# Kernel optimization log

Measured on AMD Instinct MI355X. Metric: run time of the kernel, lower is better.

## Reference

```python
import jax, jax.numpy as jnp
import numpy as np

B = 1024          # batch
IMG_IN = 4096     # raw visual feature dim
AUD_IN = 1024     # raw audio feature dim
ENC = 1024        # encoder output dim
S = 3             # multi-scale branches (768 = 3*256 in out_layer)
D = 256           # MmFA feature dim (hardcoded in module)
OUT1 = 512
LAT = 128         # minus_one_dim
NCLS = 10
NORM = 1.0 / np.sqrt(256.0)  # note: original applies this AFTER softmax


def setup_inputs() -> dict:
    key = jax.random.key(0)
    ks = jax.random.split(key, 16)
    n = lambda k, shape, s=0.02: jax.random.normal(k, shape, dtype=jnp.float32) * s
    return dict(
        img=jax.random.normal(ks[0], (B, IMG_IN), dtype=jnp.float32),
        audio=jax.random.normal(ks[1], (B, AUD_IN), dtype=jnp.float32),
        vis_W=n(ks[2], (ENC, IMG_IN)), vis_b=jnp.zeros((ENC,), jnp.float32),
        aud_W=n(ks[3], (ENC, AUD_IN)), aud_b=jnp.zeros((ENC,), jnp.float32),
        msv_W=n(ks[4], (S, D, ENC)), msv_b=jnp.zeros((S, D), jnp.float32),
        msa_W=n(ks[5], (S, D, ENC)), msa_b=jnp.zeros((S, D), jnp.float32),
        mmfa_W=n(ks[6], (8, D, D)),  # q_v,q_a,k_v,k_a,w1,w2,w3,w4
        mmfa_b=jnp.zeros((8, D), jnp.float32),
        bil_W=n(ks[7], (D, D, D)),   # nn.Bilinear(256,256,256,bias=False)
        t_c=jnp.ones((), jnp.float32),
        out_W1=n(ks[8], (OUT1, S * D)), out_b1=jnp.zeros((OUT1,), jnp.float32),
        out_W2=n(ks[9], (LAT, OUT1)), out_b2=jnp.zeros((LAT,), jnp.float32),
        clsv_W1=n(ks[10], (32, LAT)), clsv_W2=n(ks[11], (NCLS, 32)),
        clsa_W1=n(ks[12], (32, LAT)), clsa_W2=n(ks[13], (NCLS, 32)),
    )


def _mmfa(x_v, x_a, W, b, bil_W, t_c):
    # x_v, x_a: [B, S, D]
    lin = lambda i, x: jnp.einsum('bsd,kd->bsk', x, W[i]) + b[i]
    q_v, q_a, k_v, k_a = lin(0, x_v), lin(1, x_a), lin(2, x_v), lin(3, x_a)
    # faithful to source: softmax first, then scale by 1/sqrt(dim_k)
    att = lambda q, k: jax.nn.softmax(jnp.einsum('bsd,btd->bst', q, k), axis=-1) * NORM
    alpha_va = jnp.einsum('bst,btd->bsd', att(q_v, k_a), x_a)
    alpha_v = jnp.einsum('bst,btd->bsd', att(q_v, k_v), x_v)
    alpha_av = jnp.einsum('bst,btd->bsd', att(q_a, k_v), x_v)
    alpha_a = jnp.einsum('bst,btd->bsd', att(q_a, k_a), x_a)
    c_va = jax.nn.sigmoid((lin(4, alpha_va) + lin(5, alpha_v)) * alpha_v)
    c_av = jax.nn.sigmoid((lin(6, alpha_av) + lin(7, alpha_a)) * alpha_a)
    j = jax.nn.sigmoid(jnp.einsum('bsi,oij,bsj->bso', c_va, bil_W, c_av))
    return t_c * j * x_v + (1.0 - j) * x_a


def reference(img, audio, vis_W, vis_b, aud_W, aud_b, msv_W, msv_b, msa_W, msa_b,
              mmfa_W, mmfa_b, bil_W, t_c, out_W1, out_b1, out_W2, out_b2,
              clsv_W1, clsv_W2, clsa_W1, clsa_W2):
    vis = jax.nn.relu(img @ vis_W.T + vis_b)       # [B, ENC]
    aud = jax.nn.relu(audio @ aud_W.T + aud_b)     # [B, ENC]
    # reconstructed MultiScale_Modal_Net: 3 parallel Linear(ENC->D)+ReLU -> [B,S,D]
    v_ms = jax.nn.relu(jnp.einsum('bd,skd->bsk', vis, msv_W) + msv_b)
    a_ms = jax.nn.relu(jnp.einsum('bd,skd->bsk', aud, msa_W) + msa_b)
    M1 = _mmfa(v_ms, a_ms, mmfa_W, mmfa_b, bil_W, t_c)
    M2 = _mmfa(M1 * v_ms, M1 * a_ms, mmfa_W, mmfa_b, bil_W, t_c)
    ov = (M2 * v_ms).reshape(img.shape[0], -1)     # [B, 768]
    oa = (M2 * a_ms).reshape(img.shape[0], -1)
    # out_layer (dropout = identity in eval)
    fv = jax.nn.relu(ov @ out_W1.T + out_b1) @ out_W2.T + out_b2   # [B, 128]
    fa = jax.nn.relu(oa @ out_W1.T + out_b1) @ out_W2.T + out_b2
    pv = jax.nn.relu(fv @ clsv_W1.T) @ clsv_W2.T                   # [B, 10]
    pa = jax.nn.relu(fa @ clsa_W1.T) @ clsa_W2.T
    return (fv, fa, pv, pa)
```

## Files before the change

kernel.cpp:

```cpp
#include <hip/hip_runtime.h>
#include <math.h>


typedef short short8   __attribute__((ext_vector_type(8)));
typedef float floatx4  __attribute__((ext_vector_type(4)));

constexpr float NORM = 0.0625f;

__device__ __forceinline__ unsigned short f2bf(float f) {
    union { float f; unsigned int u; } v; v.f = f;
    unsigned int r = v.u + 0x7fffu + ((v.u >> 16) & 1u);
    return (unsigned short)(r >> 16);
}
__device__ __forceinline__ float bf2f(unsigned short s) {
    union { unsigned int u; float f; } v; v.u = ((unsigned int)s) << 16;
    return v.f;
}

template<int ACT>
__global__ __launch_bounds__(256)
void gemm_mfma(const float* __restrict__ A, const unsigned short* __restrict__ W,
               const float* __restrict__ bias, float* __restrict__ C,
               int M, int N, int K)
{
    __shared__ short sA[64][72];
    __shared__ short sW[64][72];
    const int tid  = threadIdx.x;
    const int wave = tid >> 6, lane = tid & 63;
    const int quad = lane >> 4, l15 = lane & 15;
    const int m0 = blockIdx.y * 64, n0 = blockIdx.x * 64;
    const int mw = (wave & 1) * 32, nw = (wave >> 1) * 32;
    const int srow = tid >> 2, sseg = tid & 3;

    floatx4 P[2][2];
    #pragma unroll
    for (int f = 0; f < 2; f++)
        #pragma unroll
        for (int g = 0; g < 2; g++)
            P[f][g] = (floatx4){0.f, 0.f, 0.f, 0.f};

    for (int k0 = 0; k0 < K; k0 += 64) {
        const float* ap = A + (size_t)(m0 + srow) * K + k0 + sseg * 16;
        float4 a0 = *(const float4*)(ap);
        float4 a1 = *(const float4*)(ap + 4);
        float4 a2 = *(const float4*)(ap + 8);
        float4 a3 = *(const float4*)(ap + 12);
        union { unsigned short s[8]; short8 v; } p0, p1;
        p0.s[0] = f2bf(a0.x); p0.s[1] = f2bf(a0.y); p0.s[2] = f2bf(a0.z); p0.s[3] = f2bf(a0.w);
        p0.s[4] = f2bf(a1.x); p0.s[5] = f2bf(a1.y); p0.s[6] = f2bf(a1.z); p0.s[7] = f2bf(a1.w);
        p1.s[0] = f2bf(a2.x); p1.s[1] = f2bf(a2.y); p1.s[2] = f2bf(a2.z); p1.s[3] = f2bf(a2.w);
        p1.s[4] = f2bf(a3.x); p1.s[5] = f2bf(a3.y); p1.s[6] = f2bf(a3.z); p1.s[7] = f2bf(a3.w);
        *(short8*)&sA[srow][sseg * 16]     = p0.v;
        *(short8*)&sA[srow][sseg * 16 + 8] = p1.v;
        const unsigned short* wp = W + (size_t)(n0 + srow) * K + k0 + sseg * 16;
        *(short8*)&sW[srow][sseg * 16]     = *(const short8*)wp;
        *(short8*)&sW[srow][sseg * 16 + 8] = *(const short8*)(wp + 8);
        __syncthreads();
        #pragma unroll
        for (int kh = 0; kh < 2; kh++) {
            short8 af[2], wf[2];
            af[0] = *(short8*)&sA[mw + l15][kh * 32 + quad * 8];
            af[1] = *(short8*)&sA[mw + 16 + l15][kh * 32 + quad * 8];
            wf[0] = *(short8*)&sW[nw + l15][kh * 32 + quad * 8];
            wf[1] = *(short8*)&sW[nw + 16 + l15][kh * 32 + quad * 8];
            #pragma unroll
            for (int f = 0; f < 2; f++)
                #pragma unroll
                for (int g = 0; g < 2; g++)
                    P[f][g] = __builtin_amdgcn_mfma_f32_16x16x32_bf16(af[f], wf[g], P[f][g], 0, 0, 0);
        }
        __syncthreads();
    }
    #pragma unroll
    for (int f = 0; f < 2; f++)
        #pragma unroll
        for (int g = 0; g < 2; g++)
            #pragma unroll
            for (int r = 0; r < 4; r++) {
                int m = m0 + mw + 16 * f + quad * 4 + r;
                int n = n0 + nw + 16 * g + l15;
                float v = P[f][g][r] + bias[n];
                if (ACT) v = fmaxf(v, 0.f);
                C[(size_t)m * N + n] = v;
            }
}

__global__ __launch_bounds__(256)
void gemm_sigm(const float* __restrict__ A, const unsigned short* __restrict__ W,
               const float* __restrict__ bias, const float* __restrict__ al,
               unsigned short* __restrict__ Cbf, int M, int N, int K)
{
    __shared__ short sA[64][72];
    __shared__ short sW[64][72];
    const int tid  = threadIdx.x;
    const int wave = tid >> 6, lane = tid & 63;
    const int quad = lane >> 4, l15 = lane & 15;
    const int m0 = blockIdx.y * 64, n0 = blockIdx.x * 64;
    const int mw = (wave & 1) * 32, nw = (wave >> 1) * 32;
    const int srow = tid >> 2, sseg = tid & 3;

    floatx4 P[2][2];
    #pragma unroll
    for (int f = 0; f < 2; f++)
        #pragma unroll
        for (int g = 0; g < 2; g++)
            P[f][g] = (floatx4){0.f, 0.f, 0.f, 0.f};

    for (int k0 = 0; k0 < K; k0 += 64) {
        const float* ap = A + (size_t)(m0 + srow) * K + k0 + sseg * 16;
        float4 a0 = *(const float4*)(ap);
        float4 a1 = *(const float4*)(ap + 4);
        float4 a2 = *(const float4*)(ap + 8);
        float4 a3 = *(const float4*)(ap + 12);
        union { unsigned short s[8]; short8 v; } p0, p1;
        p0.s[0] = f2bf(a0.x); p0.s[1] = f2bf(a0.y); p0.s[2] = f2bf(a0.z); p0.s[3] = f2bf(a0.w);
        p0.s[4] = f2bf(a1.x); p0.s[5] = f2bf(a1.y); p0.s[6] = f2bf(a1.z); p0.s[7] = f2bf(a1.w);
        p1.s[0] = f2bf(a2.x); p1.s[1] = f2bf(a2.y); p1.s[2] = f2bf(a2.z); p1.s[3] = f2bf(a2.w);
        p1.s[4] = f2bf(a3.x); p1.s[5] = f2bf(a3.y); p1.s[6] = f2bf(a3.z); p1.s[7] = f2bf(a3.w);
        *(short8*)&sA[srow][sseg * 16]     = p0.v;
        *(short8*)&sA[srow][sseg * 16 + 8] = p1.v;
        const unsigned short* wp = W + (size_t)(n0 + srow) * K + k0 + sseg * 16;
        *(short8*)&sW[srow][sseg * 16]     = *(const short8*)wp;
        *(short8*)&sW[srow][sseg * 16 + 8] = *(const short8*)(wp + 8);
        __syncthreads();
        #pragma unroll
        for (int kh = 0; kh < 2; kh++) {
            short8 af[2], wf[2];
            af[0] = *(short8*)&sA[mw + l15][kh * 32 + quad * 8];
            af[1] = *(short8*)&sA[mw + 16 + l15][kh * 32 + quad * 8];
            wf[0] = *(short8*)&sW[nw + l15][kh * 32 + quad * 8];
            wf[1] = *(short8*)&sW[nw + 16 + l15][kh * 32 + quad * 8];
            #pragma unroll
            for (int f = 0; f < 2; f++)
                #pragma unroll
                for (int g = 0; g < 2; g++)
                    P[f][g] = __builtin_amdgcn_mfma_f32_16x16x32_bf16(af[f], wf[g], P[f][g], 0, 0, 0);
        }
        __syncthreads();
    }
    #pragma unroll
    for (int f = 0; f < 2; f++)
        #pragma unroll
        for (int g = 0; g < 2; g++)
            #pragma unroll
            for (int r = 0; r < 4; r++) {
                int m = m0 + mw + 16 * f + quad * 4 + r;
                int n = n0 + nw + 16 * g + l15;
                float v = P[f][g][r] + bias[n];
                float a = al[(size_t)m * 512 + 256 + n];
                Cbf[(size_t)m * N + n] = f2bf(1.f / (1.f + expf(-v * a)));
            }
}

template<int ACT>
__global__ __launch_bounds__(256)
void gemm_bt(const float* __restrict__ A, const float* __restrict__ W,
             const float* __restrict__ bias, float* __restrict__ C,
             int M, int N, int K)
{
    __shared__ __align__(16) float sA[32][68];
    __shared__ __align__(16) float sB[32][68];
    const int tid = threadIdx.x;
    const int m0 = blockIdx.y * 64;
    const int n0 = blockIdx.x * 64;
    const int tx = tid & 15;
    const int ty = tid >> 4;
    const int kk = tid & 31;
    const int rr = tid >> 5;
    float acc[4][4] = {};
    for (int k0 = 0; k0 < K; k0 += 32) {
        #pragma unroll
        for (int p = 0; p < 8; p++) {
            int mm = rr + p * 8;
            int m  = m0 + mm;
            int k  = k0 + kk;
            sA[kk][mm] = (m < M && k < K) ? A[(size_t)m * K + k] : 0.f;
        }
        #pragma unroll
        for (int p = 0; p < 8; p++) {
            int nn = rr + p * 8;
            int n  = n0 + nn;
            int k  = k0 + kk;
            sB[kk][nn] = (n < N && k < K) ? W[(size_t)n * K + k] : 0.f;
        }
        __syncthreads();
        #pragma unroll
        for (int q = 0; q < 32; q++) {
            float av[4], bv[4];
            #pragma unroll
            for (int i = 0; i < 4; i++) av[i] = sA[q][ty * 4 + i];
            #pragma unroll
            for (int j = 0; j < 4; j++) bv[j] = sB[q][tx * 4 + j];
            #pragma unroll
            for (int i = 0; i < 4; i++)
                #pragma unroll
                for (int j = 0; j < 4; j++)
                    acc[i][j] += av[i] * bv[j];
        }
        __syncthreads();
    }
    #pragma unroll
    for (int i = 0; i < 4; i++) {
        int m = m0 + ty * 4 + i;
        if (m >= M) continue;
        #pragma unroll
        for (int j = 0; j < 4; j++) {
            int n = n0 + tx * 4 + j;
            if (n >= N) continue;
            float v = acc[i][j];
            if (bias) v += bias[n];
            if (ACT) v = fmaxf(v, 0.f);
            C[(size_t)m * N + n] = v;
        }
    }
}

__global__ __launch_bounds__(256)
void conv_w(const float* __restrict__ src, unsigned short* __restrict__ dst, int n)
{
    int i = (blockIdx.x * 256 + threadIdx.x) * 8;
    if (i + 7 < n) {
        float4 a = *(const float4*)(src + i);
        float4 b = *(const float4*)(src + i + 4);
        union { unsigned short s[8]; uint4 v; } o;
        o.s[0] = f2bf(a.x); o.s[1] = f2bf(a.y); o.s[2] = f2bf(a.z); o.s[3] = f2bf(a.w);
        o.s[4] = f2bf(b.x); o.s[5] = f2bf(b.y); o.s[6] = f2bf(b.z); o.s[7] = f2bf(b.w);
        *(uint4*)(dst + i) = o.v;
    }
}

__global__ __launch_bounds__(256)
void pack_kcat(const float* __restrict__ mW, unsigned short* __restrict__ Wcva,
               unsigned short* __restrict__ Wcav)
{
    int i = blockIdx.x * 256 + threadIdx.x;
    int row = i >> 8, col = i & 255;
    Wcva[row * 512 + col]       = f2bf(mW[4 * 65536 + i]);
    Wcva[row * 512 + 256 + col] = f2bf(mW[5 * 65536 + i]);
    Wcav[row * 512 + col]       = f2bf(mW[6 * 65536 + i]);
    Wcav[row * 512 + 256 + col] = f2bf(mW[7 * 65536 + i]);
}

__global__ __launch_bounds__(256)
void pack_bias(const float* __restrict__ mb, float* __restrict__ bqkv,
               float* __restrict__ bqka, float* __restrict__ bcva,
               float* __restrict__ bcav)
{
    int i = blockIdx.x * 256 + threadIdx.x;
    int c = i & 255;
    bqkv[i] = mb[(i < 256 ? 0 : 512) + c];
    bqka[i] = mb[(i < 256 ? 256 : 768) + c];
    if (i < 256) {
        bcva[i] = mb[4 * 256 + i] + mb[5 * 256 + i];
        bcav[i] = mb[6 * 256 + i] + mb[7 * 256 + i];
    }
}

__global__ __launch_bounds__(512, 4)
void bilinear_col(const unsigned short* __restrict__ cav,
                  const unsigned short* __restrict__ cva,
                  const float* __restrict__ Wf,
                  float* __restrict__ outT)
{
    __shared__ short sA[64][264];
    __shared__ float sRed[8][64];
    const int tid  = threadIdx.x;
    const int wave = tid >> 6, lane = tid & 63;
    const int quad = lane >> 4, l15 = lane & 15;
    const int o     = blockIdx.x;
    const int mbase = blockIdx.y * 1536;
    const int i0    = wave * 32;

    short8 Wr[2][8];
    {
        const float* wo = Wf + (size_t)o * 65536;
        #pragma unroll
        for (int f = 0; f < 2; f++) {
            const float* wrow = wo + (size_t)(i0 + 16 * f + l15) * 256 + quad * 8;
            #pragma unroll
            for (int s = 0; s < 8; s++) {
                float4 lo = *(const float4*)(wrow + s * 32);
                float4 hi = *(const float4*)(wrow + s * 32 + 4);
                union { unsigned short u[8]; short8 v; } p;
                p.u[0] = f2bf(lo.x); p.u[1] = f2bf(lo.y); p.u[2] = f2bf(lo.z); p.u[3] = f2bf(lo.w);
                p.u[4] = f2bf(hi.x); p.u[5] = f2bf(hi.y); p.u[6] = f2bf(hi.z); p.u[7] = f2bf(hi.w);
                Wr[f][s] = p.v;
            }
        }
    }

    const int srow = tid >> 3, sseg = tid & 7;
    for (int ms = 0; ms < 24; ms++) {
        const int m0 = mbase + ms * 64;
        __syncthreads();
        {
            const unsigned short* src = cav + (size_t)(m0 + srow) * 256 + sseg * 32;
            #pragma unroll
            for (int u = 0; u < 4; u++)
                *(short8*)&sA[srow][sseg * 32 + u * 8] = *(const short8*)(src + u * 8);
        }
        __syncthreads();

        uint2 raws[2][4];
        #pragma unroll
        for (int g = 0; g < 4; g++)
            #pragma unroll
            for (int f = 0; f < 2; f++)
                raws[f][g] = *(const uint2*)(cva + (size_t)(m0 + 16 * g + l15) * 256
                                                  + i0 + 16 * f + 4 * quad);

        floatx4 P2[2][4];
        #pragma unroll
        for (int f = 0; f < 2; f++)
            #pragma unroll
            for (int g = 0; g < 4; g++)
                P2[f][g] = (floatx4){0.f, 0.f, 0.f, 0.f};

        #pragma unroll
        for (int s = 0; s < 8; s++) {
            short8 bg[4];
            #pragma unroll
            for (int g = 0; g < 4; g++)
                bg[g] = *(const short8*)&sA[16 * g + l15][s * 32 + quad * 8];
            #pragma unroll
            for (int f = 0; f < 2; f++)
                #pragma unroll
                for (int g = 0; g < 4; g++)
                    P2[f][g] = __builtin_amdgcn_mfma_f32_16x16x32_bf16(Wr[f][s], bg[g], P2[f][g], 0, 0, 0);
        }

        float T[4] = {0.f, 0.f, 0.f, 0.f};
        #pragma unroll
        for (int g = 0; g < 4; g++)
            #pragma unroll
            for (int f = 0; f < 2; f++) {
                uint2 raw = raws[f][g];
                T[g] += bf2f((unsigned short)(raw.x & 0xffff)) * P2[f][g][0]
                      + bf2f((unsigned short)(raw.x >> 16))    * P2[f][g][1]
                      + bf2f((unsigned short)(raw.y & 0xffff)) * P2[f][g][2]
                      + bf2f((unsigned short)(raw.y >> 16))    * P2[f][g][3];
            }
        #pragma unroll
        for (int g = 0; g < 4; g++) {
            T[g] += __shfl_xor(T[g], 16);
            T[g] += __shfl_xor(T[g], 32);
        }
        if (quad == 0) {
            #pragma unroll
            for (int g = 0; g < 4; g++)
                sRed[wave][16 * g + l15] = T[g];
        }
        __syncthreads();
        if (tid < 64) {
            float acc = sRed[0][tid] + sRed[1][tid] + sRed[2][tid] + sRed[3][tid]
                      + sRed[4][tid] + sRed[5][tid] + sRed[6][tid] + sRed[7][tid];
            outT[(size_t)o * 3072 + m0 + tid] = acc;
        }
    }
}

__global__ __launch_bounds__(256)
void attn_packed(const float* __restrict__ qkv, const float* __restrict__ qka,
                 const float* __restrict__ xv, const float* __restrict__ xa,
                 float* __restrict__ al_v, float* __restrict__ al_a)
{
    const int b    = blockIdx.x;
    const int tid  = threadIdx.x;
    const int wave = tid >> 6;
    const int lane = tid & 63;
    __shared__ float att[4][3][3];
    const size_t b512 = (size_t)b * 1536;
    const size_t b768 = (size_t)b * 768;
    const float* Qs[4] = {qkv, qkv, qka, qka};
    const float* Ks[4] = {qka + 256, qkv + 256, qkv + 256, qka + 256};
    const float* Xs[4] = {xa, xv, xv, xa};
    float*       Os[4] = {al_v, al_v + 256, al_a, al_a + 256};
    const float* q = Qs[wave] + b512;
    const float* k = Ks[wave] + b512;
    float part[9] = {};
    for (int d = lane; d < 256; d += 64) {
        float q0 = q[d], q1 = q[512 + d], q2 = q[1024 + d];
        float k0 = k[d], k1 = k[512 + d], k2 = k[1024 + d];
        part[0] += q0 * k0; part[1] += q0 * k1; part[2] += q0 * k2;
        part[3] += q1 * k0; part[4] += q1 * k1; part[5] += q1 * k2;
        part[6] += q2 * k0; part[7] += q2 * k1; part[8] += q2 * k2;
    }
    #pragma unroll
    for (int off = 32; off > 0; off >>= 1)
        #pragma unroll
        for (int i = 0; i < 9; i++) part[i] += __shfl_down(part[i], off);
    if (lane == 0) {
        #pragma unroll
        for (int s = 0; s < 3; s++) {
            float a0 = part[s * 3], a1 = part[s * 3 + 1], a2 = part[s * 3 + 2];
            float mx = fmaxf(a0, fmaxf(a1, a2));
            float e0 = expf(a0 - mx), e1 = expf(a1 - mx), e2 = expf(a2 - mx);
            float inv = NORM / (e0 + e1 + e2);
            att[wave][s][0] = e0 * inv;
            att[wave][s][1] = e1 * inv;
            att[wave][s][2] = e2 * inv;
        }
    }
    __syncthreads();
    const int d = tid;
    #pragma unroll
    for (int w = 0; w < 4; w++) {
        const float* x = Xs[w] + b768;
        float x0 = x[d], x1 = x[256 + d], x2 = x[512 + d];
        float* o = Os[w] + b512;
        #pragma unroll
        for (int s = 0; s < 3; s++)
            o[s * 512 + d] = att[w][s][0] * x0 + att[w][s][1] * x1 + att[w][s][2] * x2;
    }
}

__global__ void ew_mix(const float* __restrict__ logitsT, const float* __restrict__ xv,
                       const float* __restrict__ xa, const float* __restrict__ bv,
                       const float* __restrict__ ba, const float* __restrict__ tc,
                       float* __restrict__ outv, float* __restrict__ outa, int n)
{
    int i = blockIdx.x * 256 + threadIdx.x;
    if (i < n) {
        int m = i >> 8, o = i & 255;
        float j = 1.f / (1.f + expf(-logitsT[(size_t)o * 3072 + m]));
        float M = tc[0] * j * xv[i] + (1.f - j) * xa[i];
        outv[i] = M * bv[i];
        outa[i] = M * ba[i];
    }
}

extern "C" void kernel_launch(void* const* d_in, const int* in_sizes, int n_in,
                              void* d_out, int out_size, void* d_ws, size_t ws_size,
                              hipStream_t stream)
{
    const float* img    = (const float*)d_in[0];
    const float* audio  = (const float*)d_in[1];
    const float* vis_W  = (const float*)d_in[2];
    const float* vis_b  = (const float*)d_in[3];
    const float* aud_W  = (const float*)d_in[4];
    const float* aud_b  = (const float*)d_in[5];
    const float* msv_W  = (const float*)d_in[6];
    const float* msv_b  = (const float*)d_in[7];
    const float* msa_W  = (const float*)d_in[8];
    const float* msa_b  = (const float*)d_in[9];
    const float* mmfa_W = (const float*)d_in[10];
    const float* mmfa_b = (const float*)d_in[11];
    const float* bil_W  = (const float*)d_in[12];
    const float* t_c    = (const float*)d_in[13];
    const float* out_W1 = (const float*)d_in[14];
    const float* out_b1 = (const float*)d_in[15];
    const float* out_W2 = (const float*)d_in[16];
    const float* out_b2 = (const float*)d_in[17];
    const float* clsv_W1 = (const float*)d_in[18];
    const float* clsv_W2 = (const float*)d_in[19];
    const float* clsa_W1 = (const float*)d_in[20];
    const float* clsa_W2 = (const float*)d_in[21];
    float* out = (float*)d_out;
    float* ws  = (float*)d_ws;

    constexpr size_t SD = 3072 * 256;
    float* S = ws;
    unsigned short* visbf = (unsigned short*)(S + 2097152);
    unsigned short* audbf = (unsigned short*)(S + 4194304);
    unsigned short* msvbf = (unsigned short*)(S + 4718592);
    unsigned short* msabf = (unsigned short*)(S + 5111808);
    float* vis  = S;
    float* aud  = S + 1048576;
    float* qkv  = S;
    float* qka  = S + 1572864;
    float* al_v = S + 3145728;
    float* al_a = S + 4718592;
    float* ovb  = S;
    float* oab  = S + SD;
    float* hv   = S + 2 * SD;
    float* hc   = S + 2 * SD + 524288;
    unsigned short* W1bf = (unsigned short*)(S + 2 * SD + 557056);
    unsigned short* W2bf = W1bf + 393216;
    float* P = ws + 8388608;
    float* v_ms    = P;
    float* a_ms    = P + SD;
    float* x_v2    = P + 2 * SD;
    float* x_a2    = P + 3 * SD;
    float* logitsT = P + 4 * SD;
    unsigned short* c_va = (unsigned short*)(P + 5 * SD);
    unsigned short* c_av = (unsigned short*)(P + 5 * SD + SD / 2);
    unsigned short* Wqkv = (unsigned short*)(P + 6 * SD);
    unsigned short* Wqka = Wqkv + 131072;
    unsigned short* Wcva = Wqka + 131072;
    unsigned short* Wcav = Wcva + 131072;
    float* bqkv = P + 6 * SD + 262144;
    float* bqka = bqkv + 512;
    float* bcva = bqka + 512;
    float* bcav = bcva + 256;

    auto gmf = [&](const float* A, const unsigned short* W, const float* bias,
                   float* C, int M, int N, int K, int act) {
        dim3 g(N / 64, M / 64);
        if (act) gemm_mfma<1><<<g, 256, 0, stream>>>(A, W, bias, C, M, N, K);
        else     gemm_mfma<0><<<g, 256, 0, stream>>>(A, W, bias, C, M, N, K);
    };
    auto gbt = [&](const float* A, const float* W, const float* bias, float* C,
                   int M, int N, int K, int act) {
        dim3 g((N + 63) / 64, (M + 63) / 64);
        if (act) gemm_bt<1><<<g, 256, 0, stream>>>(A, W, bias, C, M, N, K);
        else     gemm_bt<0><<<g, 256, 0, stream>>>(A, W, bias, C, M, N, K);
    };

    conv_w<<<2048, 256, 0, stream>>>(vis_W, visbf, 4194304);
    conv_w<<<512,  256, 0, stream>>>(aud_W, audbf, 1048576);
    conv_w<<<384,  256, 0, stream>>>(msv_W, msvbf, 786432);
    conv_w<<<384,  256, 0, stream>>>(msa_W, msabf, 786432);
    conv_w<<<32, 256, 0, stream>>>(mmfa_W + 0 * 65536, Wqkv, 65536);
    conv_w<<<32, 256, 0, stream>>>(mmfa_W + 2 * 65536, Wqkv + 65536, 65536);
    conv_w<<<32, 256, 0, stream>>>(mmfa_W + 1 * 65536, Wqka, 65536);
    conv_w<<<32, 256, 0, stream>>>(mmfa_W + 3 * 65536, Wqka + 65536, 65536);
    pack_kcat<<<256, 256, 0, stream>>>(mmfa_W, Wcva, Wcav);
    pack_bias<<<2, 256, 0, stream>>>(mmfa_b, bqkv, bqka, bcva, bcav);

    gmf(img,   visbf, vis_b, vis, 1024, 1024, 4096, 1);
    gmf(audio, audbf, aud_b, aud, 1024, 1024, 1024, 1);
    gmf(vis, msvbf, msv_b, v_ms, 1024, 768, 1024, 1);
    gmf(aud, msabf, msa_b, a_ms, 1024, 768, 1024, 1);

    const int EW_N = (int)SD;
    const int EW_G = (EW_N + 255) / 256;

    auto mmfa = [&](const float* xv, const float* xa, float* outv, float* outa) {
        gmf(xv, Wqkv, bqkv, qkv, 3072, 512, 256, 0);
        gmf(xa, Wqka, bqka, qka, 3072, 512, 256, 0);
        attn_packed<<<1024, 256, 0, stream>>>(qkv, qka, xv, xa, al_v, al_a);
        gemm_sigm<<<dim3(4, 48), 256, 0, stream>>>(al_v, Wcva, bcva, al_v, c_va,
                                                   3072, 256, 512);
        gemm_sigm<<<dim3(4, 48), 256, 0, stream>>>(al_a, Wcav, bcav, al_a, c_av,
                                                   3072, 256, 512);
        bilinear_col<<<dim3(256, 2), 512, 0, stream>>>(c_av, c_va, bil_W, logitsT);
        ew_mix<<<EW_G, 256, 0, stream>>>(logitsT, xv, xa, v_ms, a_ms, t_c,
                                         outv, outa, EW_N);
    };

    mmfa(v_ms, a_ms, x_v2, x_a2);
    mmfa(x_v2, x_a2, ovb, oab);

    float* fv = out;
    float* fa = out + 1024 * 128;
    float* pv = out + 2 * 1024 * 128;
    float* pa = pv + 1024 * 10;

    conv_w<<<192, 256, 0, stream>>>(out_W1, W1bf, 393216);
    conv_w<<<32,  256, 0, stream>>>(out_W2, W2bf, 65536);
    gmf(ovb, W1bf, out_b1, hv, 1024, 512, 768, 1);
    gmf(hv,  W2bf, out_b2, fv, 1024, 128, 512, 0);
    gmf(oab, W1bf, out_b1, hv, 1024, 512, 768, 1);
    gmf(hv,  W2bf, out_b2, fa, 1024, 128, 512, 0);

    gbt(fv, clsv_W1, nullptr, hc, 1024, 32, 128, 1);
    gbt(hc, clsv_W2, nullptr, pv, 1024, 10, 32, 0);
    gbt(fa, clsa_W1, nullptr, hc, 1024, 32, 128, 1);
    gbt(hc, clsa_W2, nullptr, pa, 1024, 10, 32, 0);

    (void)in_sizes; (void)n_in; (void)out_size; (void)ws_size;
}
```

Before: 866.4 us.

## Batch paired GEMMs via grid z, merge conversions, fuse classifier, double-buffer bilinear

Paired GEMM launches (ms projections, q/k projections, gating sigmoid GEMMs, out-layer GEMMs) are merged into single launches that pick their operands by blockIdx.z. The many weight conversion and packing kernels collapse into two launches, and the four tiny classifier GEMMs become one fused kernel. The bilinear kernel now double-buffers its shared-memory tile and defers the reduction write by one step, which drops one barrier per iteration. Together these cut launch count and idle gaps, at the cost of more complex index logic and larger shared-memory use in the bilinear kernel.

```diff
diff --git a/kernel.cpp b/kernel.cpp
--- a/kernel.cpp
+++ b/kernel.cpp
@@ -19,10 +19,18 @@
 
 template<int ACT>
 __global__ __launch_bounds__(256)
-void gemm_mfma(const float* __restrict__ A, const unsigned short* __restrict__ W,
-               const float* __restrict__ bias, float* __restrict__ C,
-               int M, int N, int K)
-{
+void gemm_mfma_z(const float* __restrict__ A0, const float* __restrict__ A1,
+                 const unsigned short* __restrict__ Wp0,
+                 const unsigned short* __restrict__ Wp1,
+                 const float* __restrict__ b0, const float* __restrict__ b1,
+                 float* __restrict__ C0, float* __restrict__ C1,
+                 int M, int N, int K)
+{
+    const float* A = blockIdx.z ? A1 : A0;
+    const unsigned short* W = blockIdx.z ? Wp1 : Wp0;
+    const float* bias = blockIdx.z ? b1 : b0;
+    float* C = blockIdx.z ? C1 : C0;
+
     __shared__ short sA[64][72];
     __shared__ short sW[64][72];
     const int tid  = threadIdx.x;
@@ -86,10 +94,18 @@
 }
 
 __global__ __launch_bounds__(256)
-void gemm_sigm(const float* __restrict__ A, const unsigned short* __restrict__ W,
-               const float* __restrict__ bias, const float* __restrict__ al,
-               unsigned short* __restrict__ Cbf, int M, int N, int K)
-{
+void gemm_sigm_z(const float* __restrict__ A0, const float* __restrict__ A1,
+                 const unsigned short* __restrict__ Wp0,
+                 const unsigned short* __restrict__ Wp1,
+                 const float* __restrict__ b0, const float* __restrict__ b1,
+                 unsigned short* __restrict__ O0, unsigned short* __restrict__ O1,
+                 int M, int N, int K)
+{
+    const float* A = blockIdx.z ? A1 : A0;
+    const unsigned short* W = blockIdx.z ? Wp1 : Wp0;
+    const float* bias = blockIdx.z ? b1 : b0;
+    unsigned short* Cbf = blockIdx.z ? O1 : O0;
+
     __shared__ short sA[64][72];
     __shared__ short sW[64][72];
     const int tid  = threadIdx.x;
@@ -147,112 +163,68 @@
                 int m = m0 + mw + 16 * f + quad * 4 + r;
                 int n = n0 + nw + 16 * g + l15;
                 float v = P[f][g][r] + bias[n];
-                float a = al[(size_t)m * 512 + 256 + n];
+                float a = A[(size_t)m * 512 + 256 + n];
                 Cbf[(size_t)m * N + n] = f2bf(1.f / (1.f + expf(-v * a)));
             }
 }
 
-template<int ACT>
 __global__ __launch_bounds__(256)
-void gemm_bt(const float* __restrict__ A, const float* __restrict__ W,
-             const float* __restrict__ bias, float* __restrict__ C,
-             int M, int N, int K)
-{
-    __shared__ __align__(16) float sA[32][68];
-    __shared__ __align__(16) float sB[32][68];
-    const int tid = threadIdx.x;
-    const int m0 = blockIdx.y * 64;
-    const int n0 = blockIdx.x * 64;
-    const int tx = tid & 15;
-    const int ty = tid >> 4;
-    const int kk = tid & 31;
-    const int rr = tid >> 5;
-    float acc[4][4] = {};
-    for (int k0 = 0; k0 < K; k0 += 32) {
-        #pragma unroll
-        for (int p = 0; p < 8; p++) {
-            int mm = rr + p * 8;
-            int m  = m0 + mm;
-            int k  = k0 + kk;
-            sA[kk][mm] = (m < M && k < K) ? A[(size_t)m * K + k] : 0.f;
-        }
-        #pragma unroll
-        for (int p = 0; p < 8; p++) {
-            int nn = rr + p * 8;
-            int n  = n0 + nn;
-            int k  = k0 + kk;
-            sB[kk][nn] = (n < N && k < K) ? W[(size_t)n * K + k] : 0.f;
-        }
-        __syncthreads();
-        #pragma unroll
-        for (int q = 0; q < 32; q++) {
-            float av[4], bv[4];
-            #pragma unroll
-            for (int i = 0; i < 4; i++) av[i] = sA[q][ty * 4 + i];
-            #pragma unroll
-            for (int j = 0; j < 4; j++) bv[j] = sB[q][tx * 4 + j];
-            #pragma unroll
-            for (int i = 0; i < 4; i++)
-                #pragma unroll
-                for (int j = 0; j < 4; j++)
-                    acc[i][j] += av[i] * bv[j];
-        }
-        __syncthreads();
-    }
-    #pragma unroll
-    for (int i = 0; i < 4; i++) {
-        int m = m0 + ty * 4 + i;
-        if (m >= M) continue;
-        #pragma unroll
-        for (int j = 0; j < 4; j++) {
-            int n = n0 + tx * 4 + j;
-            if (n >= N) continue;
-            float v = acc[i][j];
-            if (bias) v += bias[n];
-            if (ACT) v = fmaxf(v, 0.f);
-            C[(size_t)m * N + n] = v;
-        }
-    }
+void conv_multi(const float* __restrict__ s0, unsigned short* __restrict__ d0,
+                const float* __restrict__ s1, unsigned short* __restrict__ d1,
+                const float* __restrict__ s2, unsigned short* __restrict__ d2,
+                const float* __restrict__ s3, unsigned short* __restrict__ d3,
+                const float* __restrict__ s4, unsigned short* __restrict__ d4,
+                const float* __restrict__ s5, unsigned short* __restrict__ d5)
+{
+    long long g = ((long long)blockIdx.x * 256 + threadIdx.x) * 8;
+    const float* src; unsigned short* dst; long long off = g;
+    if      (off < 4194304)                 { src = s0; dst = d0; }
+    else if ((off = g - 4194304) < 1048576) { src = s1; dst = d1; }
+    else if ((off = g - 5242880) < 786432)  { src = s2; dst = d2; }
+    else if ((off = g - 6029312) < 786432)  { src = s3; dst = d3; }
+    else if ((off = g - 6815744) < 393216)  { src = s4; dst = d4; }
+    else if ((off = g - 7208960) < 65536)   { src = s5; dst = d5; }
+    else return;
+    float4 a = *(const float4*)(src + off);
+    float4 b = *(const float4*)(src + off + 4);
+    union { unsigned short s[8]; uint4 v; } o;
+    o.s[0] = f2bf(a.x); o.s[1] = f2bf(a.y); o.s[2] = f2bf(a.z); o.s[3] = f2bf(a.w);
+    o.s[4] = f2bf(b.x); o.s[5] = f2bf(b.y); o.s[6] = f2bf(b.z); o.s[7] = f2bf(b.w);
+    *(uint4*)(dst + off) = o.v;
 }
 
 __global__ __launch_bounds__(256)
-void conv_w(const float* __restrict__ src, unsigned short* __restrict__ dst, int n)
-{
-    int i = (blockIdx.x * 256 + threadIdx.x) * 8;
-    if (i + 7 < n) {
-        float4 a = *(const float4*)(src + i);
-        float4 b = *(const float4*)(src + i + 4);
-        union { unsigned short s[8]; uint4 v; } o;
-        o.s[0] = f2bf(a.x); o.s[1] = f2bf(a.y); o.s[2] = f2bf(a.z); o.s[3] = f2bf(a.w);
-        o.s[4] = f2bf(b.x); o.s[5] = f2bf(b.y); o.s[6] = f2bf(b.z); o.s[7] = f2bf(b.w);
-        *(uint4*)(dst + i) = o.v;
-    }
-}
-
-__global__ __launch_bounds__(256)
-void pack_kcat(const float* __restrict__ mW, unsigned short* __restrict__ Wcva,
-               unsigned short* __restrict__ Wcav)
-{
-    int i = blockIdx.x * 256 + threadIdx.x;
-    int row = i >> 8, col = i & 255;
-    Wcva[row * 512 + col]       = f2bf(mW[4 * 65536 + i]);
-    Wcva[row * 512 + 256 + col] = f2bf(mW[5 * 65536 + i]);
-    Wcav[row * 512 + col]       = f2bf(mW[6 * 65536 + i]);
-    Wcav[row * 512 + 256 + col] = f2bf(mW[7 * 65536 + i]);
-}
-
-__global__ __launch_bounds__(256)
-void pack_bias(const float* __restrict__ mb, float* __restrict__ bqkv,
-               float* __restrict__ bqka, float* __restrict__ bcva,
-               float* __restrict__ bcav)
-{
-    int i = blockIdx.x * 256 + threadIdx.x;
-    int c = i & 255;
-    bqkv[i] = mb[(i < 256 ? 0 : 512) + c];
-    bqka[i] = mb[(i < 256 ? 256 : 768) + c];
-    if (i < 256) {
-        bcva[i] = mb[4 * 256 + i] + mb[5 * 256 + i];
-        bcav[i] = mb[6 * 256 + i] + mb[7 * 256 + i];
+void pack_mmfa(const float* __restrict__ mW, const float* __restrict__ mb,
+               unsigned short* __restrict__ Wqkv, unsigned short* __restrict__ Wqka,
+               unsigned short* __restrict__ Wcva, unsigned short* __restrict__ Wcav,
+               float* __restrict__ bqkv, float* __restrict__ bqka,
+               float* __restrict__ bcva, float* __restrict__ bcav)
+{
+    int b = blockIdx.x;
+    if (b < 2048) {
+        int i = b * 256 + threadIdx.x;
+        int w = i >> 16, r = i & 65535;
+        unsigned short s = f2bf(mW[i]);
+        int row = r >> 8, col = r & 255;
+        switch (w) {
+            case 0: Wqkv[r] = s; break;
+            case 1: Wqka[r] = s; break;
+            case 2: Wqkv[65536 + r] = s; break;
+            case 3: Wqka[65536 + r] = s; break;
+            case 4: Wcva[row * 512 + col] = s; break;
+            case 5: Wcva[row * 512 + 256 + col] = s; break;
+            case 6: Wcav[row * 512 + col] = s; break;
+            case 7: Wcav[row * 512 + 256 + col] = s; break;
+        }
+    } else {
+        int i = threadIdx.x;
+        for (int t = i; t < 512; t += 256) {
+            int c = t & 255;
+            bqkv[t] = mb[(t < 256 ? 0 : 512) + c];
+            bqka[t] = mb[(t < 256 ? 256 : 768) + c];
+        }
+        bcva[i] = mb[1024 + i] + mb[1280 + i];
+        bcav[i] = mb[1536 + i] + mb[1792 + i];
     }
 }
 
@@ -262,8 +234,8 @@
                   const float* __restrict__ Wf,
                   float* __restrict__ outT)
 {
-    __shared__ short sA[64][264];
-    __shared__ float sRed[8][64];
+    __shared__ short sA[2][64][264];
+    __shared__ float sRed[2][8][64];
     const int tid  = threadIdx.x;
     const int wave = tid >> 6, lane = tid & 63;
     const int quad = lane >> 4, l15 = lane & 15;
@@ -290,72 +262,88 @@
     }
 
     const int srow = tid >> 3, sseg = tid & 7;
-    for (int ms = 0; ms < 24; ms++) {
-        const int m0 = mbase + ms * 64;
+    {
+        const unsigned short* src = cav + (size_t)(mbase + srow) * 256 + sseg * 32;
+        #pragma unroll
+        for (int u = 0; u < 4; u++)
+            *(short8*)&sA[0][srow][sseg * 32 + u * 8] = *(const short8*)(src + u * 8);
+    }
+    __syncthreads();
+
+    for (int ms = 0; ms <= 24; ms++) {
+        const int cur = ms & 1;
+        if (ms < 24) {
+            const int m0 = mbase + ms * 64;
+            const bool have_next = (ms < 23);
+            short8 stg[4];
+            if (have_next) {
+                const unsigned short* src = cav + (size_t)(m0 + 64 + srow) * 256 + sseg * 32;
+                #pragma unroll
+                for (int u = 0; u < 4; u++) stg[u] = *(const short8*)(src + u * 8);
+            }
+            uint2 raws[2][4];
+            #pragma unroll
+            for (int g = 0; g < 4; g++)
+                #pragma unroll
+                for (int f = 0; f < 2; f++)
+                    raws[f][g] = *(const uint2*)(cva + (size_t)(m0 + 16 * g + l15) * 256
+                                                      + i0 + 16 * f + 4 * quad);
+
+            floatx4 P2[2][4];
+            #pragma unroll
+            for (int f = 0; f < 2; f++)
+                #pragma unroll
+                for (int g = 0; g < 4; g++)
+                    P2[f][g] = (floatx4){0.f, 0.f, 0.f, 0.f};
+
+            #pragma unroll
+            for (int s = 0; s < 8; s++) {
+                short8 bg[4];
+                #pragma unroll
+                for (int g = 0; g < 4; g++)
+                    bg[g] = *(const short8*)&sA[cur][16 * g + l15][s * 32 + quad * 8];
+                #pragma unroll
+                for (int f = 0; f < 2; f++)
+                    #pragma unroll
+                    for (int g = 0; g < 4; g++)
+                        P2[f][g] = __builtin_amdgcn_mfma_f32_16x16x32_bf16(Wr[f][s], bg[g], P2[f][g], 0, 0, 0);
+            }
+
+            float T[4] = {0.f, 0.f, 0.f, 0.f};
+            #pragma unroll
+            for (int g = 0; g < 4; g++)
+                #pragma unroll
+                for (int f = 0; f < 2; f++) {
+                    uint2 raw = raws[f][g];
+                    T[g] += bf2f((unsigned short)(raw.x & 0xffff)) * P2[f][g][0]
+                          + bf2f((unsigned short)(raw.x >> 16))    * P2[f][g][1]
+                          + bf2f((unsigned short)(raw.y & 0xffff)) * P2[f][g][2]
+                          + bf2f((unsigned short)(raw.y >> 16))    * P2[f][g][3];
+                }
+            #pragma unroll
+            for (int g = 0; g < 4; g++) {
+                T[g] += __shfl_xor(T[g], 16);
+                T[g] += __shfl_xor(T[g], 32);
+            }
+            if (quad == 0) {
+                #pragma unroll
+                for (int g = 0; g < 4; g++)
+                    sRed[cur][wave][16 * g + l15] = T[g];
+            }
+            if (have_next) {
+                #pragma unroll
+                for (int u = 0; u < 4; u++)
+                    *(short8*)&sA[cur ^ 1][srow][sseg * 32 + u * 8] = stg[u];
+            }
+        }
+        if (ms > 0 && tid < 64) {
+            const int pb = (ms - 1) & 1;
+            float acc = sRed[pb][0][tid] + sRed[pb][1][tid] + sRed[pb][2][tid]
+                      + sRed[pb][3][tid] + sRed[pb][4][tid] + sRed[pb][5][tid]
+                      + sRed[pb][6][tid] + sRed[pb][7][tid];
+            outT[(size_t)o * 3072 + mbase + (ms - 1) * 64 + tid] = acc;
+        }
         __syncthreads();
-        {
-            const unsigned short* src = cav + (size_t)(m0 + srow) * 256 + sseg * 32;
-            #pragma unroll
-            for (int u = 0; u < 4; u++)
-                *(short8*)&sA[srow][sseg * 32 + u * 8] = *(const short8*)(src + u * 8);
-        }
-        __syncthreads();
-
-        uint2 raws[2][4];
-        #pragma unroll
-        for (int g = 0; g < 4; g++)
-            #pragma unroll
-            for (int f = 0; f < 2; f++)
-                raws[f][g] = *(const uint2*)(cva + (size_t)(m0 + 16 * g + l15) * 256
-                                                  + i0 + 16 * f + 4 * quad);
-
-        floatx4 P2[2][4];
-        #pragma unroll
-        for (int f = 0; f < 2; f++)
-            #pragma unroll
-            for (int g = 0; g < 4; g++)
-                P2[f][g] = (floatx4){0.f, 0.f, 0.f, 0.f};
-
-        #pragma unroll
-        for (int s = 0; s < 8; s++) {
-            short8 bg[4];
-            #pragma unroll
-            for (int g = 0; g < 4; g++)
-                bg[g] = *(const short8*)&sA[16 * g + l15][s * 32 + quad * 8];
-            #pragma unroll
-            for (int f = 0; f < 2; f++)
-                #pragma unroll
-                for (int g = 0; g < 4; g++)
-                    P2[f][g] = __builtin_amdgcn_mfma_f32_16x16x32_bf16(Wr[f][s], bg[g], P2[f][g], 0, 0, 0);
-        }
-
-        float T[4] = {0.f, 0.f, 0.f, 0.f};
-        #pragma unroll
-        for (int g = 0; g < 4; g++)
-            #pragma unroll
-            for (int f = 0; f < 2; f++) {
-                uint2 raw = raws[f][g];
-                T[g] += bf2f((unsigned short)(raw.x & 0xffff)) * P2[f][g][0]
-                      + bf2f((unsigned short)(raw.x >> 16))    * P2[f][g][1]
-                      + bf2f((unsigned short)(raw.y & 0xffff)) * P2[f][g][2]
-                      + bf2f((unsigned short)(raw.y >> 16))    * P2[f][g][3];
-            }
-        #pragma unroll
-        for (int g = 0; g < 4; g++) {
-            T[g] += __shfl_xor(T[g], 16);
-            T[g] += __shfl_xor(T[g], 32);
-        }
-        if (quad == 0) {
-            #pragma unroll
-            for (int g = 0; g < 4; g++)
-                sRed[wave][16 * g + l15] = T[g];
-        }
-        __syncthreads();
-        if (tid < 64) {
-            float acc = sRed[0][tid] + sRed[1][tid] + sRed[2][tid] + sRed[3][tid]
-                      + sRed[4][tid] + sRed[5][tid] + sRed[6][tid] + sRed[7][tid];
-            outT[(size_t)o * 3072 + m0 + tid] = acc;
-        }
     }
 }
 
@@ -426,6 +414,52 @@
         float M = tc[0] * j * xv[i] + (1.f - j) * xa[i];
         outv[i] = M * bv[i];
         outa[i] = M * ba[i];
+    }
+}
+
+__global__ __launch_bounds__(256)
+void cls_fused(const float* __restrict__ fv, const float* __restrict__ fa,
+               const float* __restrict__ Wv1, const float* __restrict__ Wv2,
+               const float* __restrict__ Wa1, const float* __restrict__ Wa2,
+               float* __restrict__ pv, float* __restrict__ pa)
+{
+    const int z = blockIdx.y;
+    const float* F  = z ? fa  : fv;
+    const float* W1 = z ? Wa1 : Wv1;
+    const float* W2 = z ? Wa2 : Wv2;
+    float* Pp       = z ? pa  : pv;
+    __shared__ float sX[64][132];
+    __shared__ float sW1[32][133];
+    __shared__ float sH[64][33];
+    __shared__ float sW2[320];
+    const int tid = threadIdx.x;
+    const int r0  = blockIdx.x * 64;
+    for (int u = tid; u < 64 * 32; u += 256) {
+        int row = u >> 5, seg = u & 31;
+        *(float4*)&sX[row][seg * 4] = *(const float4*)(F + (size_t)(r0 + row) * 128 + seg * 4);
+    }
+    for (int u = tid; u < 32 * 128; u += 256) {
+        int row = u >> 7, k = u & 127;
+        sW1[row][k] = W1[row * 128 + k];
+    }
+    if (tid < 80) ((float4*)sW2)[tid] = ((const float4*)W2)[tid];
+    __syncthreads();
+    const int r = tid >> 2, jg = (tid & 3) * 8;
+    float h[8] = {};
+    for (int k = 0; k < 128; k++) {
+        float x = sX[r][k];
+        #pragma unroll
+        for (int j = 0; j < 8; j++) h[j] += x * sW1[jg + j][k];
+    }
+    #pragma unroll
+    for (int j = 0; j < 8; j++) sH[r][jg + j] = fmaxf(h[j], 0.f);
+    __syncthreads();
+    for (int u = tid; u < 640; u += 256) {
+        int row = u / 10, oo = u % 10;
+        float acc = 0.f;
+        #pragma unroll
+        for (int j = 0; j < 32; j++) acc += sH[row][j] * sW2[oo * 32 + j];
+        Pp[(size_t)(r0 + row) * 10 + oo] = acc;
     }
 }
 
@@ -472,10 +506,8 @@
     float* al_a = S + 4718592;
     float* ovb  = S;
     float* oab  = S + SD;
-    float* hv   = S + 2 * SD;
-    float* hc   = S + 2 * SD + 524288;
-    unsigned short* W1bf = (unsigned short*)(S + 2 * SD + 557056);
-    unsigned short* W2bf = W1bf + 393216;
+    float* hv1  = S + 2 * SD;
+    float* hv2  = S + 2 * SD + 524288;
     float* P = ws + 8388608;
     float* v_ms    = P;
     float* a_ms    = P + SD;
@@ -492,47 +524,31 @@
     float* bqka = bqkv + 512;
     float* bcva = bqka + 512;
     float* bcav = bcva + 256;
-
-    auto gmf = [&](const float* A, const unsigned short* W, const float* bias,
-                   float* C, int M, int N, int K, int act) {
-        dim3 g(N / 64, M / 64);
-        if (act) gemm_mfma<1><<<g, 256, 0, stream>>>(A, W, bias, C, M, N, K);
-        else     gemm_mfma<0><<<g, 256, 0, stream>>>(A, W, bias, C, M, N, K);
-    };
-    auto gbt = [&](const float* A, const float* W, const float* bias, float* C,
-                   int M, int N, int K, int act) {
-        dim3 g((N + 63) / 64, (M + 63) / 64);
-        if (act) gemm_bt<1><<<g, 256, 0, stream>>>(A, W, bias, C, M, N, K);
-        else     gemm_bt<0><<<g, 256, 0, stream>>>(A, W, bias, C, M, N, K);
-    };
-
-    conv_w<<<2048, 256, 0, stream>>>(vis_W, visbf, 4194304);
-    conv_w<<<512,  256, 0, stream>>>(aud_W, audbf, 1048576);
-    conv_w<<<384,  256, 0, stream>>>(msv_W, msvbf, 786432);
-    conv_w<<<384,  256, 0, stream>>>(msa_W, msabf, 786432);
-    conv_w<<<32, 256, 0, stream>>>(mmfa_W + 0 * 65536, Wqkv, 65536);
-    conv_w<<<32, 256, 0, stream>>>(mmfa_W + 2 * 65536, Wqkv + 65536, 65536);
-    conv_w<<<32, 256, 0, stream>>>(mmfa_W + 1 * 65536, Wqka, 65536);
-    conv_w<<<32, 256, 0, stream>>>(mmfa_W + 3 * 65536, Wqka + 65536, 65536);
-    pack_kcat<<<256, 256, 0, stream>>>(mmfa_W, Wcva, Wcav);
-    pack_bias<<<2, 256, 0, stream>>>(mmfa_b, bqkv, bqka, bcva, bcav);
-
-    gmf(img,   visbf, vis_b, vis, 1024, 1024, 4096, 1);
-    gmf(audio, audbf, aud_b, aud, 1024, 1024, 1024, 1);
-    gmf(vis, msvbf, msv_b, v_ms, 1024, 768, 1024, 1);
-    gmf(aud, msabf, msa_b, a_ms, 1024, 768, 1024, 1);
+    unsigned short* W1bf = (unsigned short*)(bcav + 256);
+    unsigned short* W2bf = W1bf + 393216;
+
+    conv_multi<<<3552, 256, 0, stream>>>(vis_W, visbf, aud_W, audbf,
+                                         msv_W, msvbf, msa_W, msabf,
+                                         out_W1, W1bf, out_W2, W2bf);
+    pack_mmfa<<<2049, 256, 0, stream>>>(mmfa_W, mmfa_b, Wqkv, Wqka, Wcva, Wcav,
+                                        bqkv, bqka, bcva, bcav);
+
+    gemm_mfma_z<1><<<dim3(16, 16, 1), 256, 0, stream>>>(
+        img, img, visbf, visbf, vis_b, vis_b, vis, vis, 1024, 1024, 4096);
+    gemm_mfma_z<1><<<dim3(16, 16, 1), 256, 0, stream>>>(
+        audio, audio, audbf, audbf, aud_b, aud_b, aud, aud, 1024, 1024, 1024);
+    gemm_mfma_z<1><<<dim3(12, 16, 2), 256, 0, stream>>>(
+        vis, aud, msvbf, msabf, msv_b, msa_b, v_ms, a_ms, 1024, 768, 1024);
 
     const int EW_N = (int)SD;
     const int EW_G = (EW_N + 255) / 256;
 
     auto mmfa = [&](const float* xv, const float* xa, float* outv, float* outa) {
-        gmf(xv, Wqkv, bqkv, qkv, 3072, 512, 256, 0);
-        gmf(xa, Wqka, bqka, qka, 3072, 512, 256, 0);
+        gemm_mfma_z<0><<<dim3(8, 48, 2), 256, 0, stream>>>(
+            xv, xa, Wqkv, Wqka, bqkv, bqka, qkv, qka, 3072, 512, 256);
         attn_packed<<<1024, 256, 0, stream>>>(qkv, qka, xv, xa, al_v, al_a);
-        gemm_sigm<<<dim3(4, 48), 256, 0, stream>>>(al_v, Wcva, bcva, al_v, c_va,
-                                                   3072, 256, 512);
-        gemm_sigm<<<dim3(4, 48), 256, 0, stream>>>(al_a, Wcav, bcav, al_a, c_av,
-                                                   3072, 256, 512);
+        gemm_sigm_z<<<dim3(4, 48, 2), 256, 0, stream>>>(
+            al_v, al_a, Wcva, Wcav, bcva, bcav, c_va, c_av, 3072, 256, 512);
         bilinear_col<<<dim3(256, 2), 512, 0, stream>>>(c_av, c_va, bil_W, logitsT);
         ew_mix<<<EW_G, 256, 0, stream>>>(logitsT, xv, xa, v_ms, a_ms, t_c,
                                          outv, outa, EW_N);
@@ -546,17 +562,12 @@
     float* pv = out + 2 * 1024 * 128;
     float* pa = pv + 1024 * 10;
 
-    conv_w<<<192, 256, 0, stream>>>(out_W1, W1bf, 393216);
-    conv_w<<<32,  256, 0, stream>>>(out_W2, W2bf, 65536);
-    gmf(ovb, W1bf, out_b1, hv, 1024, 512, 768, 1);
-    gmf(hv,  W2bf, out_b2, fv, 1024, 128, 512, 0);
-    gmf(oab, W1bf, out_b1, hv, 1024, 512, 768, 1);
-    gmf(hv,  W2bf, out_b2, fa, 1024, 128, 512, 0);
-
-    gbt(fv, clsv_W1, nullptr, hc, 1024, 32, 128, 1);
-    gbt(hc, clsv_W2, nullptr, pv, 1024, 10, 32, 0);
-    gbt(fa, clsa_W1, nullptr, hc, 1024, 32, 128, 1);
-    gbt(hc, clsa_W2, nullptr, pa, 1024, 10, 32, 0);
+    gemm_mfma_z<1><<<dim3(8, 16, 2), 256, 0, stream>>>(
+        ovb, oab, W1bf, W1bf, out_b1, out_b1, hv1, hv2, 1024, 512, 768);
+    gemm_mfma_z<0><<<dim3(2, 16, 2), 256, 0, stream>>>(
+        hv1, hv2, W2bf, W2bf, out_b2, out_b2, fv, fa, 1024, 128, 512);
+    cls_fused<<<dim3(16, 2), 256, 0, stream>>>(fv, fa, clsv_W1, clsv_W2,
+                                               clsa_W1, clsa_W2, pv, pa);
 
     (void)in_sizes; (void)n_in; (void)out_size; (void)ws_size;
 }
```

New measurement: 872.3 us. About the same (+0.7%).
